# Kernel tuning notes

Hardware: AMD Instinct MI355X
Metric: run time of the kernel (lower is better)

The kernel has to match this reference:

```python
import jax, jax.numpy as jnp
import numpy as np

NUM_HEADS = 8
LN_EPS = 1e-8


def setup_inputs() -> dict:
    key = jax.random.key(0)
    ks = jax.random.split(key, 10)
    B, Sq, Sk, D, U = 8, 1024, 1024, 512, 512
    s = 1.0 / np.sqrt(D)
    return {
        "queries": jax.random.normal(ks[0], (B, Sq, D), jnp.float32),
        "keys": jax.random.normal(ks[1], (B, Sk, D), jnp.float32),
        "Wq": jax.random.normal(ks[2], (D, U), jnp.float32) * s,
        "bq": jnp.zeros((U,), jnp.float32),
        "Wk": jax.random.normal(ks[3], (D, U), jnp.float32) * s,
        "bk": jnp.zeros((U,), jnp.float32),
        "Wv": jax.random.normal(ks[4], (D, U), jnp.float32) * s,
        "bv": jnp.zeros((U,), jnp.float32),
        "gamma": jnp.ones((U,), jnp.float32),
        "beta": jnp.zeros((U,), jnp.float32),
    }


def reference(queries, keys, Wq, bq, Wk, bk, Wv, bv, gamma, beta):
    H = NUM_HEADS
    B, Sq, _ = queries.shape
    Sk = keys.shape[1]
    U = Wq.shape[1]
    Dh = U // H

    # ReLU-activated Q/K/V projections
    Q = jax.nn.relu(queries @ Wq + bq)   # [B,Sq,U]
    K = jax.nn.relu(keys @ Wk + bk)      # [B,Sk,U]
    V = jax.nn.relu(keys @ Wv + bv)      # [B,Sk,U]

    # split_heads: concat(split(x, H, -1), 0) == head-major [H,B,S,Dh]
    Qh = Q.reshape(B, Sq, H, Dh).transpose(2, 0, 1, 3)
    Kh = K.reshape(B, Sk, H, Dh).transpose(2, 0, 1, 3)
    Vh = V.reshape(B, Sk, H, Dh).transpose(2, 0, 1, 3)

    scores = jnp.einsum('hbqd,hbkd->hbqk', Qh, Kh) / jnp.sqrt(
        jnp.asarray(Dh, scores_dtype := Qh.dtype))
    attn = jax.nn.softmax(scores, axis=-1)

    # post-softmax query mask: zero rows where sum(|q|)==0 ([B,Sq,1] bcast)
    qmask = (jnp.sum(jnp.abs(queries), axis=-1, keepdims=True) > 0)
    attn = attn * qmask.astype(attn.dtype)[None]  # [1,B,Sq,1] -> [H,B,Sq,Sk]

    out = jnp.einsum('hbqk,hbkd->hbqd', attn, Vh)  # [H,B,Sq,Dh]
    # merge_heads: inverse of split_heads
    out = out.transpose(1, 2, 0, 3).reshape(B, Sq, U)

    out = out + queries  # residual

    # LayerNorm over last axis (keras default), eps=1e-8
    mu = jnp.mean(out, axis=-1, keepdims=True)
    var = jnp.mean(jnp.square(out - mu), axis=-1, keepdims=True)
    return gamma * (out - mu) * jax.lax.rsqrt(var + LN_EPS) + beta
```

## Files before the change

### kernel.cpp

```cpp
#include <hip/hip_runtime.h>
#include <stdint.h>

#define ROWS 8192
#define UDIM 512
#define SEQ  1024
#define NH   8
#define DH   64
#define SCALE 0.125f
#define LOG2E 1.44269504f
#define SC_Q (SCALE * LOG2E)

typedef unsigned short u16;
typedef __bf16 bf16_t;
typedef bf16_t bf16x8 __attribute__((ext_vector_type(8)));
typedef float f32x4 __attribute__((ext_vector_type(4)));
typedef float f32x16 __attribute__((ext_vector_type(16)));

__device__ __forceinline__ u16 f2bf(float f) {
    union { float f; uint32_t u; } v; v.f = f;
    uint32_t r = v.u + 0x7FFFu + ((v.u >> 16) & 1u);
    return (u16)(r >> 16);
}

__device__ __forceinline__ float bf2f(u16 b) {
    union { uint32_t u; float f; } v; v.u = ((uint32_t)b) << 16;
    return v.f;
}

__device__ __forceinline__ uint32_t pk_bf16(float a, float b) {
#if __has_builtin(__builtin_amdgcn_cvt_pk_bf16_f32)
    typedef __bf16 bf16x2_t __attribute__((ext_vector_type(2)));
    bf16x2_t r = __builtin_amdgcn_cvt_pk_bf16_f32(a, b);
    union { bf16x2_t v; uint32_t u; } c; c.v = r;
    return c.u;
#else
    return (uint32_t)f2bf(a) | ((uint32_t)f2bf(b) << 16);
#endif
}

__device__ __forceinline__ void async_ld16(u16* lds, const u16* g) {
    __builtin_amdgcn_global_load_lds((const __attribute__((address_space(1))) void*)g,
                                     (__attribute__((address_space(3))) void*)lds, 16, 0, 0);
}

__global__ void convqk_kernel(const float* __restrict__ q, const float* __restrict__ k,
                              u16* __restrict__ qb, u16* __restrict__ kb) {
    int w = threadIdx.x >> 6, lane = threadIdx.x & 63;
    int row = blockIdx.x * 4 + w;
    const float* src = (blockIdx.y == 0) ? q : k;
    u16* dst = (blockIdx.y == 0) ? qb : kb;
    const float4* s4 = (const float4*)(src + (size_t)row * UDIM);
    ushort4* o4 = (ushort4*)(dst + (size_t)row * UDIM);
    for (int j = 0; j < 2; j++) {
        float4 v = s4[j * 64 + lane];
        ushort4 b;
        b.x = f2bf(v.x); b.y = f2bf(v.y); b.z = f2bf(v.z); b.w = f2bf(v.w);
        o4[j * 64 + lane] = b;
    }
}

__global__ void transposeW_kernel(const float* __restrict__ Wq, const float* __restrict__ Wk,
                                  const float* __restrict__ Wv, u16* __restrict__ Wqt,
                                  u16* __restrict__ Wkt, u16* __restrict__ Wvt) {
    const float* in = (blockIdx.z == 0) ? Wq : (blockIdx.z == 1) ? Wk : Wv;
    u16* out = (blockIdx.z == 0) ? Wqt : (blockIdx.z == 1) ? Wkt : Wvt;
    __shared__ float tile[32][33];
    int k0 = blockIdx.y * 32, n0 = blockIdx.x * 32;
    int tx = threadIdx.x & 31, ty = threadIdx.x >> 5;
    for (int r = ty; r < 32; r += 8)
        tile[r][tx] = in[(size_t)(k0 + r) * UDIM + n0 + tx];
    __syncthreads();
    for (int r = ty; r < 32; r += 8)
        out[(size_t)(n0 + r) * UDIM + k0 + tx] = f2bf(tile[tx][r]);
}

#define CPAD 136
__global__ __launch_bounds__(256, 3) void proj_kernel(
    const u16* __restrict__ qb, const u16* __restrict__ kb,
    const u16* __restrict__ Wqt, const u16* __restrict__ Wkt, const u16* __restrict__ Wvt,
    const float* __restrict__ bq, const float* __restrict__ bk, const float* __restrict__ bv,
    u16* __restrict__ Qp, u16* __restrict__ Kp, u16* __restrict__ Vtp)
{
    const int z = blockIdx.z;
    const u16* A = (z == 0) ? qb : kb;
    const u16* W = (z == 0) ? Wqt : (z == 1) ? Wkt : Wvt;
    const float* bias = (z == 0) ? bq : (z == 1) ? bk : bv;

    __shared__ u16 smem[128 * CPAD];
    u16* c_s = smem;

    const int t = threadIdx.x;
    const int lane = t & 63, w = t >> 6;
    const int quad = lane >> 4, l15 = lane & 15;
    const int m0 = blockIdx.x * 128;
    const int n0 = blockIdx.y * 128;

    const int r0 = t >> 2;
    const int s0 = ((t & 3) ^ ((r0 >> 1) & 3)) * 8;
    const u16* Ag0 = &A[(size_t)(m0 + r0) * 512 + s0];
    const u16* Ag1 = Ag0 + (size_t)64 * 512;
    const u16* Wg0 = &W[(size_t)(n0 + r0) * 512 + s0];
    const u16* Wg1 = Wg0 + (size_t)64 * 512;
    u16* al0[2] = { &smem[0 + t * 8],     &smem[4096 + t * 8] };
    u16* al1[2] = { &smem[0 + (t + 256) * 8], &smem[4096 + (t + 256) * 8] };
    u16* bl0[2] = { &smem[8192 + t * 8],      &smem[12288 + t * 8] };
    u16* bl1[2] = { &smem[8192 + (t + 256) * 8], &smem[12288 + (t + 256) * 8] };

    int aoff[2], boff[8];
    for (int mi = 0; mi < 2; mi++) {
        int row = w * 32 + mi * 16 + l15;
        aoff[mi] = row * 32 + (quad ^ ((row >> 1) & 3)) * 8;
    }
    for (int ni = 0; ni < 8; ni++) {
        int row = ni * 16 + l15;
        boff[ni] = row * 32 + (quad ^ ((row >> 1) & 3)) * 8;
    }

    f32x4 acc[2][8];
    for (int mi = 0; mi < 2; mi++)
        for (int ni = 0; ni < 8; ni++)
            acc[mi][ni] = (f32x4){0.f, 0.f, 0.f, 0.f};

    async_ld16(al0[0], Ag0);  async_ld16(al1[0], Ag1);
    async_ld16(bl0[0], Wg0);  async_ld16(bl1[0], Wg1);
    Ag0 += 32; Ag1 += 32; Wg0 += 32; Wg1 += 32;
    __syncthreads();

    for (int kt = 0; kt < 16; kt++) {
        const int cur = kt & 1, nxt = cur ^ 1;
        if (kt < 15) {
            async_ld16(al0[nxt], Ag0);  async_ld16(al1[nxt], Ag1);
            async_ld16(bl0[nxt], Wg0);  async_ld16(bl1[nxt], Wg1);
            Ag0 += 32; Ag1 += 32; Wg0 += 32; Wg1 += 32;
        }
        const int ab = cur ? 4096 : 0, bb = cur ? 12288 : 8192;
        bf16x8 af[2], bf[8];
        for (int mi = 0; mi < 2; mi++) af[mi] = *(const bf16x8*)&smem[ab + aoff[mi]];
        for (int ni = 0; ni < 8; ni++) bf[ni] = *(const bf16x8*)&smem[bb + boff[ni]];
        for (int mi = 0; mi < 2; mi++)
            for (int ni = 0; ni < 8; ni++)
                acc[mi][ni] = __builtin_amdgcn_mfma_f32_16x16x32_bf16(af[mi], bf[ni], acc[mi][ni], 0, 0, 0);
        __syncthreads();
    }

    const float qscale = (z == 0) ? SC_Q : 1.f;
    float bvl[8];
    for (int ni = 0; ni < 8; ni++) bvl[ni] = bias[n0 + ni * 16 + l15];
    for (int mi = 0; mi < 2; mi++)
        for (int ni = 0; ni < 8; ni++)
            for (int r = 0; r < 4; r++)
                acc[mi][ni][r] = fmaxf(acc[mi][ni][r] + bvl[ni], 0.f) * qscale;

    if (z < 2) {
        for (int mi = 0; mi < 2; mi++)
            for (int ni = 0; ni < 8; ni++)
                for (int r = 0; r < 4; r++)
                    c_s[(w * 32 + mi * 16 + quad * 4 + r) * CPAD + ni * 16 + l15] =
                        f2bf(acc[mi][ni][r]);
        __syncthreads();
        u16* outp = (z == 0) ? Qp : Kp;
        for (int j = 0; j < 8; j++) {
            int c = t + j * 256;
            int mrow = c >> 4, col8 = c & 15;
            uint4 d = *(const uint4*)&c_s[mrow * CPAD + col8 * 8];
            *(uint4*)&outp[(size_t)(m0 + mrow) * 512 + n0 + col8 * 8] = d;
        }
    } else {
        for (int mi = 0; mi < 2; mi++)
            for (int ni = 0; ni < 8; ni++) {
                uint2 pk;
                pk.x = pk_bf16(acc[mi][ni][0], acc[mi][ni][1]);
                pk.y = pk_bf16(acc[mi][ni][2], acc[mi][ni][3]);
                *(uint2*)&c_s[(ni * 16 + l15) * CPAD + w * 32 + mi * 16 + quad * 4] = pk;
            }
        __syncthreads();
        const int bb2 = m0 >> 10, sk0 = m0 & 1023;
        for (int j = 0; j < 8; j++) {
            int c = t + j * 256;
            int nrow = c >> 4, col8 = c & 15;
            uint4 d = *(const uint4*)&c_s[nrow * CPAD + col8 * 8];
            *(uint4*)&Vtp[(size_t)(bb2 * 512 + n0 + nrow) * 1024 + sk0 + col8 * 8] = d;
        }
    }
}

__global__ __launch_bounds__(256, 4) void attn_kernel(
    const u16* __restrict__ Qb, const u16* __restrict__ Kb, const u16* __restrict__ Vt,
    u16* __restrict__ Obf)
{
    __shared__ u16 k_s[2][64 * 64];
    __shared__ u16 v_s[2][64 * 64];
    __shared__ u16 p_s[64 * 64];

    const int t = threadIdx.x, lane = t & 63, w = t >> 6;
    const int l31 = lane & 31, half = lane >> 5;
    const int wh = w & 1;
    const int wq = w >> 1;
    const int fid = blockIdx.x;
    const int xcd = fid & 7, j = fid >> 3;
    const int hb = xcd * 8 + (j & 7);
    const int qt = j >> 3;
    const int h = hb & 7, b = hb >> 3;
    const int q0 = qt * 64;

    const int r0 = t >> 3;
    const int s0 = ((t & 7) ^ (r0 & 7)) * 8;
    const u16* kg0 = &Kb[(size_t)(b * 1024 + r0) * 512 + h * 64 + s0];
    const u16* kg1 = kg0 + (size_t)32 * 512;
    const u16* vg0 = &Vt[(size_t)(b * 512 + h * 64 + r0) * 1024 + s0];
    const u16* vg1 = vg0 + (size_t)32 * 1024;
    u16* kd0[2] = { &k_s[0][t * 8], &k_s[1][t * 8] };
    u16* kd1[2] = { &k_s[0][(t + 256) * 8], &k_s[1][(t + 256) * 8] };
    u16* vd0[2] = { &v_s[0][t * 8], &v_s[1][t * 8] };
    u16* vd1[2] = { &v_s[0][(t + 256) * 8], &v_s[1][(t + 256) * 8] };

    bf16x8 bqf[4];
    {
        int qrow = b * 1024 + q0 + 32 * wq + l31;
        for (int tk = 0; tk < 4; tk++)
            bqf[tk] = *(const bf16x8*)&Qb[(size_t)qrow * 512 + h * 64 + tk * 16 + half * 8];
    }

    int koff[4];
    {
        int row = 32 * wh + l31;
        for (int tk = 0; tk < 4; tk++)
            koff[tk] = row * 64 + (((2 * tk + half) ^ (row & 7))) * 8;
    }
    const int prow = 32 * wq + l31;
    int pwoff[4], proff[4];
    for (int g = 0; g < 4; g++)
        pwoff[g] = prow * 64 + ((4 * wh + g) ^ (prow & 7)) * 8 + half * 4;
    for (int tk = 0; tk < 4; tk++)
        proff[tk] = prow * 64 + ((2 * tk + half) ^ (prow & 7)) * 8;

    float l_lane = 0.f;
    f32x16 o_acc = (f32x16){0.f,0.f,0.f,0.f,0.f,0.f,0.f,0.f,
                            0.f,0.f,0.f,0.f,0.f,0.f,0.f,0.f};

    async_ld16(kd0[0], kg0);  async_ld16(kd1[0], kg1);
    async_ld16(vd0[0], vg0);  async_ld16(vd1[0], vg1);
    kg0 += (size_t)64 * 512; kg1 += (size_t)64 * 512;
    vg0 += 64; vg1 += 64;
    __syncthreads();

    for (int it = 0; it < 16; it++) {
        const int cur = it & 1, nxt = cur ^ 1;

        if (it < 15) {
            async_ld16(kd0[nxt], kg0);  async_ld16(kd1[nxt], kg1);
            async_ld16(vd0[nxt], vg0);  async_ld16(vd1[nxt], vg1);
            kg0 += (size_t)64 * 512; kg1 += (size_t)64 * 512;
            vg0 += 64; vg1 += 64;
        }

        bf16x8 ak[4], av[4];
        for (int tk = 0; tk < 4; tk++) {
            ak[tk] = *(const bf16x8*)&k_s[cur][koff[tk]];
            av[tk] = *(const bf16x8*)&v_s[cur][koff[tk]];
        }

        f32x16 st = (f32x16){0.f,0.f,0.f,0.f,0.f,0.f,0.f,0.f,
                             0.f,0.f,0.f,0.f,0.f,0.f,0.f,0.f};
        for (int tk = 0; tk < 4; tk++)
            st = __builtin_amdgcn_mfma_f32_32x32x16_bf16(ak[tk], bqf[tk], st, 0, 0, 0);

        for (int g = 0; g < 4; g++) {
            float p0 = exp2f(st[4 * g + 0]);
            float p1 = exp2f(st[4 * g + 1]);
            float p2 = exp2f(st[4 * g + 2]);
            float p3 = exp2f(st[4 * g + 3]);
            l_lane += (p0 + p1) + (p2 + p3);
            uint2 pk;
            pk.x = pk_bf16(p0, p1);
            pk.y = pk_bf16(p2, p3);
            *(uint2*)&p_s[pwoff[g]] = pk;
        }

        __syncthreads();

        for (int tk = 0; tk < 4; tk++) {
            bf16x8 bp = *(const bf16x8*)&p_s[proff[tk]];
            o_acc = __builtin_amdgcn_mfma_f32_32x32x16_bf16(av[tk], bp, o_acc, 0, 0, 0);
        }

        if (it < 15)
            __syncthreads();
    }

    __syncthreads();
    float l2 = l_lane + __shfl_xor(l_lane, 32, 64);
    float* lbuf = (float*)&k_s[0][0];
    if (lane < 32) lbuf[w * 32 + l31] = l2;
    __syncthreads();
    float ltot = lbuf[w * 32 + l31] + lbuf[(w ^ 1) * 32 + l31];
    float inv = 1.f / ltot;

    for (int g = 0; g < 4; g++) {
        uint2 pk;
        pk.x = pk_bf16(o_acc[4 * g + 0] * inv, o_acc[4 * g + 1] * inv);
        pk.y = pk_bf16(o_acc[4 * g + 2] * inv, o_acc[4 * g + 3] * inv);
        *(uint2*)&p_s[pwoff[g]] = pk;
    }
    __syncthreads();
    for (int rnd = 0; rnd < 2; rnd++) {
        int c = t + rnd * 256;
        int row = c >> 3, slot = c & 7;
        int phys = slot ^ (row & 7);
        uint4 d4 = *(const uint4*)&p_s[row * 64 + phys * 8];
        *(uint4*)&Obf[(size_t)(b * 1024 + q0 + row) * 512 + h * 64 + slot * 8] = d4;
    }
}

__global__ void ln_kernel(const u16* __restrict__ O, const float* __restrict__ q,
                          const float* __restrict__ gamma, const float* __restrict__ beta,
                          float* __restrict__ out)
{
    int w = threadIdx.x >> 6, lane = threadIdx.x & 63;
    int row = blockIdx.x * 4 + w;
    const float4* q4 = (const float4*)(q + (size_t)row * UDIM);
    float4* o4 = (float4*)(out + (size_t)row * UDIM);

    float4 qq[2];
    float am = 0.f;
    for (int j = 0; j < 2; j++) {
        qq[j] = q4[2 * lane + j];
        am += fabsf(qq[j].x) + fabsf(qq[j].y) + fabsf(qq[j].z) + fabsf(qq[j].w);
    }
    uint4 ov = *(const uint4*)&O[(size_t)row * UDIM + lane * 8];
    float oo[8];
    oo[0] = bf2f((u16)(ov.x & 0xFFFF));  oo[1] = bf2f((u16)(ov.x >> 16));
    oo[2] = bf2f((u16)(ov.y & 0xFFFF));  oo[3] = bf2f((u16)(ov.y >> 16));
    oo[4] = bf2f((u16)(ov.z & 0xFFFF));  oo[5] = bf2f((u16)(ov.z >> 16));
    oo[6] = bf2f((u16)(ov.w & 0xFFFF));  oo[7] = bf2f((u16)(ov.w >> 16));

    for (int off = 32; off; off >>= 1) am += __shfl_xor(am, off, 64);
    float mask = (am > 0.f) ? 1.f : 0.f;

    float4 x[2];
    float s = 0.f, ss = 0.f;
    for (int j = 0; j < 2; j++) {
        float4 v;
        v.x = oo[4 * j + 0] * mask + qq[j].x;
        v.y = oo[4 * j + 1] * mask + qq[j].y;
        v.z = oo[4 * j + 2] * mask + qq[j].z;
        v.w = oo[4 * j + 3] * mask + qq[j].w;
        x[j] = v;
        s += v.x + v.y + v.z + v.w;
        ss += v.x * v.x + v.y * v.y + v.z * v.z + v.w * v.w;
    }
    for (int off = 32; off; off >>= 1) {
        s += __shfl_xor(s, off, 64);
        ss += __shfl_xor(ss, off, 64);
    }
    float mu = s * (1.f / 512.f);
    float var = ss * (1.f / 512.f) - mu * mu;
    float rs = rsqrtf(var + 1e-8f);
    for (int j = 0; j < 2; j++) {
        float4 g = ((const float4*)gamma)[2 * lane + j];
        float4 bb = ((const float4*)beta)[2 * lane + j];
        float4 v;
        v.x = g.x * (x[j].x - mu) * rs + bb.x;
        v.y = g.y * (x[j].y - mu) * rs + bb.y;
        v.z = g.z * (x[j].z - mu) * rs + bb.z;
        v.w = g.w * (x[j].w - mu) * rs + bb.w;
        o4[2 * lane + j] = v;
    }
}

extern "C" void kernel_launch(void* const* d_in, const int* in_sizes, int n_in,
                              void* d_out, int out_size, void* d_ws, size_t ws_size,
                              hipStream_t stream)
{
    const float* queries = (const float*)d_in[0];
    const float* keys    = (const float*)d_in[1];
    const float* Wq      = (const float*)d_in[2];
    const float* bq      = (const float*)d_in[3];
    const float* Wk      = (const float*)d_in[4];
    const float* bk      = (const float*)d_in[5];
    const float* Wv      = (const float*)d_in[6];
    const float* bv      = (const float*)d_in[7];
    const float* gamma   = (const float*)d_in[8];
    const float* beta    = (const float*)d_in[9];
    float* out = (float*)d_out;

    char* ws = (char*)d_ws;
    size_t off = 0;
    auto alloc = [&](size_t bytes) {
        void* p = ws + off;
        off += (bytes + 255) & ~(size_t)255;
        return p;
    };
    u16* qb   = (u16*)alloc((size_t)ROWS * UDIM * 2);
    u16* kb   = (u16*)alloc((size_t)ROWS * UDIM * 2);
    u16* Wqt  = (u16*)alloc((size_t)UDIM * UDIM * 2);
    u16* Wkt  = (u16*)alloc((size_t)UDIM * UDIM * 2);
    u16* Wvt  = (u16*)alloc((size_t)UDIM * UDIM * 2);
    u16* Qp   = (u16*)alloc((size_t)ROWS * UDIM * 2);
    u16* Kp   = (u16*)alloc((size_t)ROWS * UDIM * 2);
    u16* Vtp  = (u16*)alloc((size_t)ROWS * UDIM * 2);
    u16* Obf  = (u16*)alloc((size_t)ROWS * UDIM * 2);

    convqk_kernel<<<dim3(ROWS / 4, 2), 256, 0, stream>>>(queries, keys, qb, kb);
    transposeW_kernel<<<dim3(16, 16, 3), 256, 0, stream>>>(Wq, Wk, Wv, Wqt, Wkt, Wvt);
    proj_kernel<<<dim3(64, 4, 3), 256, 0, stream>>>(qb, kb, Wqt, Wkt, Wvt, bq, bk, bv, Qp, Kp, Vtp);
    attn_kernel<<<1024, 256, 0, stream>>>(Qp, Kp, Vtp, Obf);
    ln_kernel<<<ROWS / 4, 256, 0, stream>>>(Obf, queries, gamma, beta, out);
}
```

Measured before the change: 161.3 us.

## Fuse fp32-to-bf16 input conversion into projection GEMM and use fast exp2

Removes the separate conversion kernel and its bf16 intermediate buffers. The projection GEMM now streams fp32 activations straight into LDS with a new swizzle and packs them to bf16 when loading fragments. The attention softmax switches to the hardware exp2 builtin. The cost is double the global and LDS traffic for the A operand in the GEMM, repeated conversion work across the four N-tiles and three projections, and slightly less exp precision.

```diff
diff --git a/kernel.cpp b/kernel.cpp
--- a/kernel.cpp
+++ b/kernel.cpp
@@ -38,25 +38,17 @@
 #endif
 }
 
+__device__ __forceinline__ float fast_exp2(float x) {
+#if __has_builtin(__builtin_amdgcn_exp2f)
+    return __builtin_amdgcn_exp2f(x);
+#else
+    return exp2f(x);
+#endif
+}
+
 __device__ __forceinline__ void async_ld16(u16* lds, const u16* g) {
     __builtin_amdgcn_global_load_lds((const __attribute__((address_space(1))) void*)g,
                                      (__attribute__((address_space(3))) void*)lds, 16, 0, 0);
-}
-
-__global__ void convqk_kernel(const float* __restrict__ q, const float* __restrict__ k,
-                              u16* __restrict__ qb, u16* __restrict__ kb) {
-    int w = threadIdx.x >> 6, lane = threadIdx.x & 63;
-    int row = blockIdx.x * 4 + w;
-    const float* src = (blockIdx.y == 0) ? q : k;
-    u16* dst = (blockIdx.y == 0) ? qb : kb;
-    const float4* s4 = (const float4*)(src + (size_t)row * UDIM);
-    ushort4* o4 = (ushort4*)(dst + (size_t)row * UDIM);
-    for (int j = 0; j < 2; j++) {
-        float4 v = s4[j * 64 + lane];
-        ushort4 b;
-        b.x = f2bf(v.x); b.y = f2bf(v.y); b.z = f2bf(v.z); b.w = f2bf(v.w);
-        o4[j * 64 + lane] = b;
-    }
 }
 
 __global__ void transposeW_kernel(const float* __restrict__ Wq, const float* __restrict__ Wk,
@@ -76,17 +68,18 @@
 
 #define CPAD 136
 __global__ __launch_bounds__(256, 3) void proj_kernel(
-    const u16* __restrict__ qb, const u16* __restrict__ kb,
+    const float* __restrict__ queries, const float* __restrict__ keys,
     const u16* __restrict__ Wqt, const u16* __restrict__ Wkt, const u16* __restrict__ Wvt,
     const float* __restrict__ bq, const float* __restrict__ bk, const float* __restrict__ bv,
     u16* __restrict__ Qp, u16* __restrict__ Kp, u16* __restrict__ Vtp)
 {
     const int z = blockIdx.z;
-    const u16* A = (z == 0) ? qb : kb;
+    const float* A = (z == 0) ? queries : keys;
     const u16* W = (z == 0) ? Wqt : (z == 1) ? Wkt : Wvt;
     const float* bias = (z == 0) ? bq : (z == 1) ? bk : bv;
 
-    __shared__ u16 smem[128 * CPAD];
+    __shared__ u16 smem[24576];
+    float* smf = (float*)smem;
     u16* c_s = smem;
 
     const int t = threadIdx.x;
@@ -95,22 +88,34 @@
     const int m0 = blockIdx.x * 128;
     const int n0 = blockIdx.y * 128;
 
-    const int r0 = t >> 2;
-    const int s0 = ((t & 3) ^ ((r0 >> 1) & 3)) * 8;
-    const u16* Ag0 = &A[(size_t)(m0 + r0) * 512 + s0];
-    const u16* Ag1 = Ag0 + (size_t)64 * 512;
-    const u16* Wg0 = &W[(size_t)(n0 + r0) * 512 + s0];
-    const u16* Wg1 = Wg0 + (size_t)64 * 512;
-    u16* al0[2] = { &smem[0 + t * 8],     &smem[4096 + t * 8] };
-    u16* al1[2] = { &smem[0 + (t + 256) * 8], &smem[4096 + (t + 256) * 8] };
-    u16* bl0[2] = { &smem[8192 + t * 8],      &smem[12288 + t * 8] };
-    u16* bl1[2] = { &smem[8192 + (t + 256) * 8], &smem[12288 + (t + 256) * 8] };
-
-    int aoff[2], boff[8];
+    const float* Agp[4];
+    u16* Adst[4][2];
+    for (int i = 0; i < 4; i++) {
+        int c = t + i * 256;
+        int row = c >> 3, jg = (c & 7) ^ (row & 7);
+        Agp[i] = &A[(size_t)(m0 + row) * 512 + jg * 4];
+        Adst[i][0] = &smem[c * 8];
+        Adst[i][1] = &smem[8192 + c * 8];
+    }
+    const u16* Wgp[2];
+    u16* Bdst[2][2];
+    for (int i = 0; i < 2; i++) {
+        int c = t + i * 256;
+        int row = c >> 2, jg = (c & 3) ^ ((row >> 1) & 3);
+        Wgp[i] = &W[(size_t)(n0 + row) * 512 + jg * 8];
+        Bdst[i][0] = &smem[16384 + c * 8];
+        Bdst[i][1] = &smem[20480 + c * 8];
+    }
+
+    int aoffF[2][2];
     for (int mi = 0; mi < 2; mi++) {
         int row = w * 32 + mi * 16 + l15;
-        aoff[mi] = row * 32 + (quad ^ ((row >> 1) & 3)) * 8;
-    }
+        int p0 = (2 * quad) ^ (row & 7);
+        int p1 = (2 * quad + 1) ^ (row & 7);
+        aoffF[mi][0] = row * 32 + p0 * 4;
+        aoffF[mi][1] = row * 32 + p1 * 4;
+    }
+    int boff[8];
     for (int ni = 0; ni < 8; ni++) {
         int row = ni * 16 + l15;
         boff[ni] = row * 32 + (quad ^ ((row >> 1) & 3)) * 8;
@@ -121,22 +126,35 @@
         for (int ni = 0; ni < 8; ni++)
             acc[mi][ni] = (f32x4){0.f, 0.f, 0.f, 0.f};
 
-    async_ld16(al0[0], Ag0);  async_ld16(al1[0], Ag1);
-    async_ld16(bl0[0], Wg0);  async_ld16(bl1[0], Wg1);
-    Ag0 += 32; Ag1 += 32; Wg0 += 32; Wg1 += 32;
+    for (int i = 0; i < 4; i++) async_ld16(Adst[i][0], (const u16*)Agp[i]);
+    for (int i = 0; i < 2; i++) async_ld16(Bdst[i][0], Wgp[i]);
+    for (int i = 0; i < 4; i++) Agp[i] += 32;
+    for (int i = 0; i < 2; i++) Wgp[i] += 32;
     __syncthreads();
 
     for (int kt = 0; kt < 16; kt++) {
         const int cur = kt & 1, nxt = cur ^ 1;
         if (kt < 15) {
-            async_ld16(al0[nxt], Ag0);  async_ld16(al1[nxt], Ag1);
-            async_ld16(bl0[nxt], Wg0);  async_ld16(bl1[nxt], Wg1);
-            Ag0 += 32; Ag1 += 32; Wg0 += 32; Wg1 += 32;
-        }
-        const int ab = cur ? 4096 : 0, bb = cur ? 12288 : 8192;
+            for (int i = 0; i < 4; i++) async_ld16(Adst[i][nxt], (const u16*)Agp[i]);
+            for (int i = 0; i < 2; i++) async_ld16(Bdst[i][nxt], Wgp[i]);
+            for (int i = 0; i < 4; i++) Agp[i] += 32;
+            for (int i = 0; i < 2; i++) Wgp[i] += 32;
+        }
+        const int abF = cur ? 4096 : 0;
+        const int bbU = cur ? 20480 : 16384;
+
         bf16x8 af[2], bf[8];
-        for (int mi = 0; mi < 2; mi++) af[mi] = *(const bf16x8*)&smem[ab + aoff[mi]];
-        for (int ni = 0; ni < 8; ni++) bf[ni] = *(const bf16x8*)&smem[bb + boff[ni]];
+        for (int mi = 0; mi < 2; mi++) {
+            f32x4 x0 = *(const f32x4*)&smf[abF + aoffF[mi][0]];
+            f32x4 x1 = *(const f32x4*)&smf[abF + aoffF[mi][1]];
+            union { bf16x8 v; uint32_t u[4]; } pk;
+            pk.u[0] = pk_bf16(x0[0], x0[1]);
+            pk.u[1] = pk_bf16(x0[2], x0[3]);
+            pk.u[2] = pk_bf16(x1[0], x1[1]);
+            pk.u[3] = pk_bf16(x1[2], x1[3]);
+            af[mi] = pk.v;
+        }
+        for (int ni = 0; ni < 8; ni++) bf[ni] = *(const bf16x8*)&smem[bbU + boff[ni]];
         for (int mi = 0; mi < 2; mi++)
             for (int ni = 0; ni < 8; ni++)
                 acc[mi][ni] = __builtin_amdgcn_mfma_f32_16x16x32_bf16(af[mi], bf[ni], acc[mi][ni], 0, 0, 0);
@@ -266,10 +284,10 @@
             st = __builtin_amdgcn_mfma_f32_32x32x16_bf16(ak[tk], bqf[tk], st, 0, 0, 0);
 
         for (int g = 0; g < 4; g++) {
-            float p0 = exp2f(st[4 * g + 0]);
-            float p1 = exp2f(st[4 * g + 1]);
-            float p2 = exp2f(st[4 * g + 2]);
-            float p3 = exp2f(st[4 * g + 3]);
+            float p0 = fast_exp2(st[4 * g + 0]);
+            float p1 = fast_exp2(st[4 * g + 1]);
+            float p2 = fast_exp2(st[4 * g + 2]);
+            float p3 = fast_exp2(st[4 * g + 3]);
             l_lane += (p0 + p1) + (p2 + p3);
             uint2 pk;
             pk.x = pk_bf16(p0, p1);
@@ -391,8 +409,6 @@
         off += (bytes + 255) & ~(size_t)255;
         return p;
     };
-    u16* qb   = (u16*)alloc((size_t)ROWS * UDIM * 2);
-    u16* kb   = (u16*)alloc((size_t)ROWS * UDIM * 2);
     u16* Wqt  = (u16*)alloc((size_t)UDIM * UDIM * 2);
     u16* Wkt  = (u16*)alloc((size_t)UDIM * UDIM * 2);
     u16* Wvt  = (u16*)alloc((size_t)UDIM * UDIM * 2);
@@ -401,9 +417,9 @@
     u16* Vtp  = (u16*)alloc((size_t)ROWS * UDIM * 2);
     u16* Obf  = (u16*)alloc((size_t)ROWS * UDIM * 2);
 
-    convqk_kernel<<<dim3(ROWS / 4, 2), 256, 0, stream>>>(queries, keys, qb, kb);
     transposeW_kernel<<<dim3(16, 16, 3), 256, 0, stream>>>(Wq, Wk, Wv, Wqt, Wkt, Wvt);
-    proj_kernel<<<dim3(64, 4, 3), 256, 0, stream>>>(qb, kb, Wqt, Wkt, Wvt, bq, bk, bv, Qp, Kp, Vtp);
+    proj_kernel<<<dim3(64, 4, 3), 256, 0, stream>>>(queries, keys, Wqt, Wkt, Wvt,
+                                                    bq, bk, bv, Qp, Kp, Vtp);
     attn_kernel<<<1024, 256, 0, stream>>>(Qp, Kp, Vtp, Obf);
     ln_kernel<<<ROWS / 4, 256, 0, stream>>>(Obf, queries, gamma, beta, out);
 }
```

Result: faster. 151.4 us (-6.1%).
